# Optimization experiments

Hardware: AMD Instinct MI355X
Metric: run time of the kernel (lower is better)

The kernel has to match this reference:

```python
import jax, jax.numpy as jnp
import numpy as np

LEAKY_SLOPE = 0.2  # LeakyReLU(0.2) attention activation from the torch module
HEADS = 4
RATES = (10, 25)


def _prod(v):
    r = 1
    for x in v:
        r *= x
    return r


def gat_conv(x_self, x_neigh, W, a_s, a_n):
    """Single GAT aggregation layer (aggregate_method='concat').
    x_self:  [..., F_in]
    x_neigh: [..., E, F_in] (leading dims reshape-compatible with x_self)
    W: [F_in, H*D], a_s/a_n: [H, D]
    Returns [..., H*D].
    """
    H = HEADS
    D = W.shape[1] // H
    lead = x_self.shape[:-1]
    E = x_neigh.shape[-2]
    z_s = (x_self @ W).reshape(lead + (H, D))                  # [..., H, D]
    z_n = (x_neigh @ W).reshape(lead + (E, H, D))              # [..., E, H, D]
    e_s = jnp.einsum('...hd,hd->...h', z_s, a_s)               # [..., H]
    e_n = jnp.einsum('...ehd,hd->...eh', z_n, a_n)             # [..., E, H]
    logits = jax.nn.leaky_relu(e_s[..., None, :] + e_n, LEAKY_SLOPE)
    alpha = jax.nn.softmax(logits, axis=-2)                    # softmax over neighbors E
    out = jnp.einsum('...eh,...ehd->...hd', alpha, z_n)        # attention-weighted sum
    return out.reshape(lead + (H * D,))


def setup_inputs() -> dict:
    key = jax.random.key(0)
    ks = jax.random.split(key, 10)
    B, F, HID, OUT = 1024, 128, 512, 256
    s = 0.05
    return {
        'h0': jax.random.normal(ks[0], (B, F), jnp.float32),
        'h1': jax.random.normal(ks[1], (B, RATES[0], F), jnp.float32),
        'h2': jax.random.normal(ks[2], (B, RATES[0] * RATES[1], F), jnp.float32),
        'W0': jax.random.normal(ks[3], (F, HID), jnp.float32) * s,
        'a0_s': jax.random.normal(ks[4], (HEADS, HID // HEADS), jnp.float32) * s,
        'a0_n': jax.random.normal(ks[5], (HEADS, HID // HEADS), jnp.float32) * s,
        'W1': jax.random.normal(ks[6], (HID, HID), jnp.float32) * s,
        'a1_s': jax.random.normal(ks[7], (HEADS, HID // HEADS), jnp.float32) * s,
        'a1_n': jax.random.normal(ks[8], (HEADS, HID // HEADS), jnp.float32) * s,
        'W_fc': jax.random.normal(ks[9], (HID, OUT), jnp.float32) * s,
    }


def reference(h0, h1, h2, W0, a0_s, a0_n, W1, a1_s, a1_n, W_fc):
    B = h0.shape[0]
    hs = [h0, h1, h2]
    layers = [(W0, a0_s, a0_n), (W1, a1_s, a1_n)]
    depth = len(RATES)
    # hierarchical sweep: layer i is applied to levels 0..depth-i-1
    for i, (W, a_s, a_n) in enumerate(layers):
        for j in range(depth - i):
            x_self = hs[j]
            x_neigh = hs[j + 1].reshape(B, _prod(RATES[:j]), RATES[j], -1)
            hs[j] = gat_conv(x_self, x_neigh, W, a_s, a_n)
    return hs[0] @ W_fc  # final Linear (no bias, no activation)
```

## Files before the change

kernel.cpp:

```cpp
#include <hip/hip_runtime.h>

__device__ __forceinline__ void gemm_body(
    float* __restrict__ smem,
    const float* __restrict__ A, int lda,
    const float* __restrict__ B, int ldb,
    float* __restrict__ C, int ldc, int K,
    int m0, int col0) {
  float* As = smem;
  float* Bs = smem + 16 * 68;
  const int t = threadIdx.x;
  const int tn = t & 31, tm = t >> 5;
  const int lam = t >> 2, lak = (t & 3) * 4;
  const int lbk = t >> 4, lbn = (t & 15) * 8;
  float acc[8][4];
#pragma unroll
  for (int i = 0; i < 8; ++i)
#pragma unroll
    for (int j = 0; j < 4; ++j) acc[i][j] = 0.f;
  for (int k0 = 0; k0 < K; k0 += 16) {
    float4 av = *reinterpret_cast<const float4*>(A + (size_t)(m0 + lam) * lda + k0 + lak);
    As[(lak + 0) * 68 + lam] = av.x;
    As[(lak + 1) * 68 + lam] = av.y;
    As[(lak + 2) * 68 + lam] = av.z;
    As[(lak + 3) * 68 + lam] = av.w;
    const float* bp = B + (size_t)(k0 + lbk) * ldb + col0 + lbn;
    float4 b0 = *reinterpret_cast<const float4*>(bp);
    float4 b1 = *reinterpret_cast<const float4*>(bp + 4);
    float* bd = &Bs[lbk * 132 + lbn];
    bd[0] = b0.x; bd[1] = b0.y; bd[2] = b0.z; bd[3] = b0.w;
    bd[4] = b1.x; bd[5] = b1.y; bd[6] = b1.z; bd[7] = b1.w;
    __syncthreads();
#pragma unroll
    for (int kk = 0; kk < 16; ++kk) {
      float4 a0 = *reinterpret_cast<const float4*>(&As[kk * 68 + tm * 8]);
      float4 a1 = *reinterpret_cast<const float4*>(&As[kk * 68 + tm * 8 + 4]);
      float4 bv = *reinterpret_cast<const float4*>(&Bs[kk * 132 + tn * 4]);
      float a[8] = {a0.x, a0.y, a0.z, a0.w, a1.x, a1.y, a1.z, a1.w};
      float b[4] = {bv.x, bv.y, bv.z, bv.w};
#pragma unroll
      for (int i = 0; i < 8; ++i)
#pragma unroll
        for (int j = 0; j < 4; ++j) acc[i][j] = fmaf(a[i], b[j], acc[i][j]);
    }
    __syncthreads();
  }
#pragma unroll
  for (int i = 0; i < 8; ++i) {
    float* cp = C + (size_t)(m0 + tm * 8 + i) * ldc + col0 + tn * 4;
    *reinterpret_cast<float4*>(cp) =
        make_float4(acc[i][0], acc[i][1], acc[i][2], acc[i][3]);
  }
}

template <int FIN, int TPR, int E>
__device__ __forceinline__ void gat_body(
    float* __restrict__ smem,
    const float* __restrict__ xself, const float* __restrict__ xneigh,
    const float* __restrict__ waS, const float* __restrict__ waN,
    float* __restrict__ out) {
  constexpr int MR = E + 1;
  constexpr int RPP = 256 / TPR;
  constexpr int PSTR = TPR + 1;
  constexpr int G = TPR / 4;
  float* tile = smem;
  float* partial = tile + MR * FIN;
  float* logitS = partial + MR * PSTR;
  float* alpha = logitS + MR * 4;
  const int t = threadIdx.x;
  const int el = t / TPR;
  const int f0 = (t % TPR) * 4;
  float4 wn[4], ws[4];
#pragma unroll
  for (int h = 0; h < 4; ++h) {
    wn[h] = *reinterpret_cast<const float4*>(waN + h * FIN + f0);
    ws[h] = *reinterpret_cast<const float4*>(waS + h * FIN + f0);
  }
#pragma unroll
  for (int p = 0; p * RPP < MR; ++p) {
    int e = p * RPP + el;
    if (e < MR) {
      const float* src = (e < E) ? (xneigh + (size_t)e * FIN + f0) : (xself + f0);
      float4 x = *reinterpret_cast<const float4*>(src);
      *reinterpret_cast<float4*>(tile + e * FIN + f0) = x;
      float ph[4];
#pragma unroll
      for (int h = 0; h < 4; ++h) {
        float4 w = (e < E) ? wn[h] : ws[h];
        ph[h] = x.x * w.x + x.y * w.y + x.z * w.z + x.w * w.w;
      }
#pragma unroll
      for (int h = 0; h < 4; ++h) {
        ph[h] += __shfl_xor(ph[h], 1);
        ph[h] += __shfl_xor(ph[h], 2);
      }
      if ((t & 3) == 0) {
        int g = (t % TPR) >> 2;
        *reinterpret_cast<float4*>(partial + e * PSTR + g * 4) =
            make_float4(ph[0], ph[1], ph[2], ph[3]);
      }
    }
  }
  __syncthreads();
  if (t < MR * 4) {
    int e = t >> 2, h = t & 3;
    float v = 0.f;
#pragma unroll
    for (int g = 0; g < G; ++g) v += partial[e * PSTR + g * 4 + h];
    logitS[t] = v;
  }
  __syncthreads();
  if (t < 4) {
    const float es = logitS[E * 4 + t];
    float m = -1e30f;
#pragma unroll
    for (int e = 0; e < E; ++e) {
      float x = es + logitS[e * 4 + t];
      x = (x > 0.f) ? x : 0.2f * x;
      m = fmaxf(m, x);
    }
    float s = 0.f;
#pragma unroll
    for (int e = 0; e < E; ++e) {
      float x = es + logitS[e * 4 + t];
      x = (x > 0.f) ? x : 0.2f * x;
      float p = __expf(x - m);
      alpha[e * 4 + t] = p;
      s += p;
    }
    float inv = 1.f / s;
#pragma unroll
    for (int e = 0; e < E; ++e) alpha[e * 4 + t] *= inv;
  }
  __syncthreads();
  constexpr int C = FIN / 4;
  for (int o = t; o < 4 * C; o += 256) {
    int h = o / C, f = (o % C) * 4;
    float4 acc = make_float4(0.f, 0.f, 0.f, 0.f);
#pragma unroll
    for (int e = 0; e < E; ++e) {
      float a = alpha[e * 4 + h];
      float4 x = *reinterpret_cast<const float4*>(tile + e * FIN + f);
      acc.x = fmaf(a, x.x, acc.x);
      acc.y = fmaf(a, x.y, acc.y);
      acc.z = fmaf(a, x.z, acc.z);
      acc.w = fmaf(a, x.w, acc.w);
    }
    *reinterpret_cast<float4*>(out + h * FIN + f) = acc;
  }
}

__global__ void __launch_bounds__(256) prepA(
    const float* __restrict__ W0, const float* __restrict__ a0s,
    const float* __restrict__ a0n,
    const float* __restrict__ W1, const float* __restrict__ a1s,
    const float* __restrict__ a1n, const float* __restrict__ Wfc,
    float* __restrict__ wa0s, float* __restrict__ wa0n,
    float* __restrict__ wa1s, float* __restrict__ wa1n,
    float* __restrict__ T) {
  __shared__ float smem[3200];
  const int b = blockIdx.x;
  if (b < 64) {
    int h = b >> 4, mb = (b >> 1) & 7, nb = b & 1;
    gemm_body(smem, W1 + h * 128, 512, Wfc + (size_t)h * 32768, 256,
              T + (size_t)h * 131072, 256, 128, mb * 64, nb * 128);
    return;
  }
  int idx = (b - 64) * 256 + threadIdx.x;
  if (idx >= 5120) return;
  const float* W; const float* a; float* dst; int i; int FIN;
  if (idx < 512)       { W = W0; a = a0s; dst = wa0s; i = idx;        FIN = 128; }
  else if (idx < 1024) { W = W0; a = a0n; dst = wa0n; i = idx - 512;  FIN = 128; }
  else if (idx < 3072) { W = W1; a = a1s; dst = wa1s; i = idx - 1024; FIN = 512; }
  else                 { W = W1; a = a1n; dst = wa1n; i = idx - 3072; FIN = 512; }
  int f = i >> 2, h = i & 3;
  const float* wrow = W + (size_t)f * 512 + h * 128;
  const float* arow = a + h * 128;
  float v = 0.f;
#pragma unroll 8
  for (int d = 0; d < 128; ++d) v = fmaf(wrow[d], arow[d], v);
  dst[h * FIN + f] = v;
}

__global__ void __launch_bounds__(256) fusedB(
    const float* __restrict__ h0, const float* __restrict__ h1,
    const float* __restrict__ h2, const float* __restrict__ wa0s,
    const float* __restrict__ wa0n, float* __restrict__ xagg,
    const float* __restrict__ W0, const float* __restrict__ wa1s,
    const float* __restrict__ wa1n, const float* __restrict__ T,
    float* __restrict__ va1s, float* __restrict__ va1n,
    float* __restrict__ Wfinal) {
  __shared__ float smem[4390];
  const int b = blockIdx.x;
  if (b < 1024) {
    gat_body<128, 32, 10>(smem, h0 + (size_t)b * 128, h1 + (size_t)b * 1280,
                          wa0s, wa0n, xagg + (size_t)b * 512);
    return;
  }
  if (b < 11264) {
    int g = b - 1024;
    gat_body<128, 32, 25>(smem, h1 + (size_t)g * 128, h2 + (size_t)g * 3200,
                          wa0s, wa0n, xagg + (size_t)b * 512);
    return;
  }
  if (b < 11264 + 64) {
    int g = b - 11264;
    int pair = g >> 2, mb = (g >> 1) & 1, nb = g & 1;
    int h = pair >> 2, h0b = pair & 3;
    gemm_body(smem, W0 + h0b * 128, 512,
              T + (size_t)h * 131072 + (size_t)h0b * 32768, 256,
              Wfinal + (size_t)h * 131072 + (size_t)h0b * 32768, 256, 128,
              mb * 64, nb * 128);
    return;
  }
  int idx = (b - 11328) * 256 + threadIdx.x;
  if (idx >= 4096) return;
  const float* wa = (idx < 2048) ? wa1s : wa1n;
  float* dst = (idx < 2048) ? va1s : va1n;
  int i = idx & 2047;
  int h = i >> 9, h0b = (i >> 7) & 3, f = i & 127;
  const float* w0row = W0 + (size_t)f * 512 + h0b * 128;
  const float* warow = wa + h * 512 + h0b * 128;
  float v = 0.f;
#pragma unroll 8
  for (int n = 0; n < 128; ++n) v = fmaf(w0row[n], warow[n], v);
  dst[i] = v;
}

__global__ void __launch_bounds__(256) gat_layer1(
    const float* __restrict__ xagg, const float* __restrict__ vaS,
    const float* __restrict__ vaN, float* __restrict__ aggx) {
  __shared__ float smem[7135];
  const int b = blockIdx.x;
  gat_body<512, 128, 10>(smem, xagg + (size_t)b * 512,
                         xagg + (size_t)(1024 + b * 10) * 512, vaS, vaN,
                         aggx + (size_t)b * 2048);
}

__global__ void __launch_bounds__(256) gemm_ksplit(
    const float* __restrict__ A, const float* __restrict__ B,
    float* __restrict__ Cpart) {
  __shared__ float smem[3200];
  const int ks = blockIdx.z;
  gemm_body(smem, A + ks * 256, 2048, B + (size_t)ks * 65536, 256,
            Cpart + (size_t)ks * 262144, 256, 256, blockIdx.x * 64,
            blockIdx.y * 128);
}

__global__ void __launch_bounds__(256) reduce8(
    const float* __restrict__ Cpart, float* __restrict__ out) {
  int i = blockIdx.x * 256 + threadIdx.x;
  const float4* p = reinterpret_cast<const float4*>(Cpart) + i;
  float4 s = p[0];
#pragma unroll
  for (int ks = 1; ks < 8; ++ks) {
    float4 v = p[(size_t)ks * 65536];
    s.x += v.x; s.y += v.y; s.z += v.z; s.w += v.w;
  }
  reinterpret_cast<float4*>(out)[i] = s;
}

extern "C" void kernel_launch(void* const* d_in, const int* in_sizes, int n_in,
                              void* d_out, int out_size, void* d_ws, size_t ws_size,
                              hipStream_t stream) {
  const float* h0  = (const float*)d_in[0];
  const float* h1  = (const float*)d_in[1];
  const float* h2  = (const float*)d_in[2];
  const float* W0  = (const float*)d_in[3];
  const float* a0s = (const float*)d_in[4];
  const float* a0n = (const float*)d_in[5];
  const float* W1  = (const float*)d_in[6];
  const float* a1s = (const float*)d_in[7];
  const float* a1n = (const float*)d_in[8];
  const float* Wfc = (const float*)d_in[9];
  float* out = (float*)d_out;

  float* ws = (float*)d_ws;
  float* wa0s   = ws;
  float* wa0n   = wa0s + 512;
  float* wa1s   = wa0n + 512;
  float* wa1n   = wa1s + 2048;
  float* va1s   = wa1n + 2048;
  float* va1n   = va1s + 2048;
  float* T      = va1n + 2048;
  float* Wfinal = T + 524288;
  float* xaggA  = Wfinal + 524288;
  float* aggx   = xaggA + 11264 * 512;
  float* Cpart  = aggx + 2097152;

  prepA<<<84, 256, 0, stream>>>(W0, a0s, a0n, W1, a1s, a1n, Wfc,
                                wa0s, wa0n, wa1s, wa1n, T);
  fusedB<<<11344, 256, 0, stream>>>(h0, h1, h2, wa0s, wa0n, xaggA,
                                    W0, wa1s, wa1n, T, va1s, va1n, Wfinal);
  gat_layer1<<<1024, 256, 0, stream>>>(xaggA, va1s, va1n, aggx);
  gemm_ksplit<<<dim3(16, 2, 8), 256, 0, stream>>>(aggx, Wfinal, Cpart);
  reduce8<<<256, 256, 0, stream>>>(Cpart, out);
}
```

Measured before the change: 271.5 us.

## Shrink GEMM tiles, use shuffle reductions and parallel softmax in GAT body

The GEMM helper moves from 64x128 to 32x128 tiles, which doubles the block count for the weight-prep and k-split GEMMs and lowers per-thread registers. The GAT attention logits are now fully reduced with warp shuffles instead of a shared-memory partial sum. The softmax runs across 64 threads with shuffle max and sum reductions instead of 4 serial threads. The weighted aggregation uses float2 so more threads take part, and the small GEMM and vector blocks are placed first in the fused launch so they do not wait behind the GAT blocks. Together these aim to cut serial work and LDS usage per block, at the cost of more blocks and less register reuse in the GEMMs.

```diff
diff --git a/kernel.cpp b/kernel.cpp
--- a/kernel.cpp
+++ b/kernel.cpp
@@ -1,52 +1,53 @@
 #include <hip/hip_runtime.h>
 
-__device__ __forceinline__ void gemm_body(
+__device__ __forceinline__ void gemm32(
     float* __restrict__ smem,
     const float* __restrict__ A, int lda,
     const float* __restrict__ B, int ldb,
     float* __restrict__ C, int ldc, int K,
     int m0, int col0) {
   float* As = smem;
-  float* Bs = smem + 16 * 68;
+  float* Bs = smem + 16 * 36;
   const int t = threadIdx.x;
   const int tn = t & 31, tm = t >> 5;
   const int lam = t >> 2, lak = (t & 3) * 4;
   const int lbk = t >> 4, lbn = (t & 15) * 8;
-  float acc[8][4];
-#pragma unroll
-  for (int i = 0; i < 8; ++i)
+  float acc[4][4];
+#pragma unroll
+  for (int i = 0; i < 4; ++i)
 #pragma unroll
     for (int j = 0; j < 4; ++j) acc[i][j] = 0.f;
   for (int k0 = 0; k0 < K; k0 += 16) {
-    float4 av = *reinterpret_cast<const float4*>(A + (size_t)(m0 + lam) * lda + k0 + lak);
-    As[(lak + 0) * 68 + lam] = av.x;
-    As[(lak + 1) * 68 + lam] = av.y;
-    As[(lak + 2) * 68 + lam] = av.z;
-    As[(lak + 3) * 68 + lam] = av.w;
+    if (t < 128) {
+      float4 av = *reinterpret_cast<const float4*>(A + (size_t)(m0 + lam) * lda + k0 + lak);
+      As[(lak + 0) * 36 + lam] = av.x;
+      As[(lak + 1) * 36 + lam] = av.y;
+      As[(lak + 2) * 36 + lam] = av.z;
+      As[(lak + 3) * 36 + lam] = av.w;
+    }
     const float* bp = B + (size_t)(k0 + lbk) * ldb + col0 + lbn;
     float4 b0 = *reinterpret_cast<const float4*>(bp);
     float4 b1 = *reinterpret_cast<const float4*>(bp + 4);
     float* bd = &Bs[lbk * 132 + lbn];
-    bd[0] = b0.x; bd[1] = b0.y; bd[2] = b0.z; bd[3] = b0.w;
-    bd[4] = b1.x; bd[5] = b1.y; bd[6] = b1.z; bd[7] = b1.w;
+    *reinterpret_cast<float4*>(bd) = b0;
+    *reinterpret_cast<float4*>(bd + 4) = b1;
     __syncthreads();
 #pragma unroll
     for (int kk = 0; kk < 16; ++kk) {
-      float4 a0 = *reinterpret_cast<const float4*>(&As[kk * 68 + tm * 8]);
-      float4 a1 = *reinterpret_cast<const float4*>(&As[kk * 68 + tm * 8 + 4]);
-      float4 bv = *reinterpret_cast<const float4*>(&Bs[kk * 132 + tn * 4]);
-      float a[8] = {a0.x, a0.y, a0.z, a0.w, a1.x, a1.y, a1.z, a1.w};
-      float b[4] = {bv.x, bv.y, bv.z, bv.w};
-#pragma unroll
-      for (int i = 0; i < 8; ++i)
+      float4 a4 = *reinterpret_cast<const float4*>(&As[kk * 36 + tm * 4]);
+      float4 b4 = *reinterpret_cast<const float4*>(&Bs[kk * 132 + tn * 4]);
+      float a[4] = {a4.x, a4.y, a4.z, a4.w};
+      float b[4] = {b4.x, b4.y, b4.z, b4.w};
+#pragma unroll
+      for (int i = 0; i < 4; ++i)
 #pragma unroll
         for (int j = 0; j < 4; ++j) acc[i][j] = fmaf(a[i], b[j], acc[i][j]);
     }
     __syncthreads();
   }
 #pragma unroll
-  for (int i = 0; i < 8; ++i) {
-    float* cp = C + (size_t)(m0 + tm * 8 + i) * ldc + col0 + tn * 4;
+  for (int i = 0; i < 4; ++i) {
+    float* cp = C + (size_t)(m0 + tm * 4 + i) * ldc + col0 + tn * 4;
     *reinterpret_cast<float4*>(cp) =
         make_float4(acc[i][0], acc[i][1], acc[i][2], acc[i][3]);
   }
@@ -60,12 +61,10 @@
     float* __restrict__ out) {
   constexpr int MR = E + 1;
   constexpr int RPP = 256 / TPR;
-  constexpr int PSTR = TPR + 1;
-  constexpr int G = TPR / 4;
+  constexpr int PP = (TPR > 64) ? 8 : 4;
   float* tile = smem;
   float* partial = tile + MR * FIN;
-  float* logitS = partial + MR * PSTR;
-  float* alpha = logitS + MR * 4;
+  float* alpha = partial + MR * PP;
   const int t = threadIdx.x;
   const int el = t / TPR;
   const int f0 = (t % TPR) * 4;
@@ -92,60 +91,76 @@
       for (int h = 0; h < 4; ++h) {
         ph[h] += __shfl_xor(ph[h], 1);
         ph[h] += __shfl_xor(ph[h], 2);
+        ph[h] += __shfl_xor(ph[h], 4);
+        ph[h] += __shfl_xor(ph[h], 8);
+        ph[h] += __shfl_xor(ph[h], 16);
+        if constexpr (TPR > 64) ph[h] += __shfl_xor(ph[h], 32);
       }
-      if ((t & 3) == 0) {
-        int g = (t % TPR) >> 2;
-        *reinterpret_cast<float4*>(partial + e * PSTR + g * 4) =
-            make_float4(ph[0], ph[1], ph[2], ph[3]);
+      if constexpr (TPR <= 64) {
+        if ((t & (TPR - 1)) == 0)
+          *reinterpret_cast<float4*>(partial + e * 4) =
+              make_float4(ph[0], ph[1], ph[2], ph[3]);
+      } else {
+        if ((t & 63) == 0) {
+          int half = (t >> 6) & 1;
+          *reinterpret_cast<float4*>(partial + e * 8 + half * 4) =
+              make_float4(ph[0], ph[1], ph[2], ph[3]);
+        }
       }
     }
   }
   __syncthreads();
-  if (t < MR * 4) {
-    int e = t >> 2, h = t & 3;
-    float v = 0.f;
-#pragma unroll
-    for (int g = 0; g < G; ++g) v += partial[e * PSTR + g * 4 + h];
-    logitS[t] = v;
+  if (t < 64) {
+    const int h = t & 3;
+    const int e0 = t >> 2;
+    float selfl = partial[E * PP + h];
+    if constexpr (PP == 8) selfl += partial[E * PP + 4 + h];
+    float x0 = -1e30f, x1 = -1e30f;
+    if (e0 < E) {
+      float v = partial[e0 * PP + h];
+      if constexpr (PP == 8) v += partial[e0 * PP + 4 + h];
+      float x = selfl + v;
+      x0 = (x > 0.f) ? x : 0.2f * x;
+    }
+    if constexpr (E > 16) {
+      if (e0 + 16 < E) {
+        float v = partial[(e0 + 16) * PP + h];
+        if constexpr (PP == 8) v += partial[(e0 + 16) * PP + 4 + h];
+        float x = selfl + v;
+        x1 = (x > 0.f) ? x : 0.2f * x;
+      }
+    }
+    float m = fmaxf(x0, x1);
+    m = fmaxf(m, __shfl_xor(m, 4));
+    m = fmaxf(m, __shfl_xor(m, 8));
+    m = fmaxf(m, __shfl_xor(m, 16));
+    m = fmaxf(m, __shfl_xor(m, 32));
+    float p0 = (e0 < E) ? __expf(x0 - m) : 0.f;
+    float p1 = 0.f;
+    if constexpr (E > 16) p1 = (e0 + 16 < E) ? __expf(x1 - m) : 0.f;
+    float s = p0 + p1;
+    s += __shfl_xor(s, 4);
+    s += __shfl_xor(s, 8);
+    s += __shfl_xor(s, 16);
+    s += __shfl_xor(s, 32);
+    float inv = 1.f / s;
+    if (e0 < E) alpha[e0 * 4 + h] = p0 * inv;
+    if constexpr (E > 16)
+      if (e0 + 16 < E) alpha[(e0 + 16) * 4 + h] = p1 * inv;
   }
   __syncthreads();
-  if (t < 4) {
-    const float es = logitS[E * 4 + t];
-    float m = -1e30f;
-#pragma unroll
-    for (int e = 0; e < E; ++e) {
-      float x = es + logitS[e * 4 + t];
-      x = (x > 0.f) ? x : 0.2f * x;
-      m = fmaxf(m, x);
-    }
-    float s = 0.f;
-#pragma unroll
-    for (int e = 0; e < E; ++e) {
-      float x = es + logitS[e * 4 + t];
-      x = (x > 0.f) ? x : 0.2f * x;
-      float p = __expf(x - m);
-      alpha[e * 4 + t] = p;
-      s += p;
-    }
-    float inv = 1.f / s;
-#pragma unroll
-    for (int e = 0; e < E; ++e) alpha[e * 4 + t] *= inv;
-  }
-  __syncthreads();
-  constexpr int C = FIN / 4;
-  for (int o = t; o < 4 * C; o += 256) {
-    int h = o / C, f = (o % C) * 4;
-    float4 acc = make_float4(0.f, 0.f, 0.f, 0.f);
+  constexpr int C2 = FIN / 2;
+  for (int o = t; o < 4 * C2; o += 256) {
+    int h = o / C2, f = (o % C2) * 2;
+    float2 acc = make_float2(0.f, 0.f);
 #pragma unroll
     for (int e = 0; e < E; ++e) {
       float a = alpha[e * 4 + h];
-      float4 x = *reinterpret_cast<const float4*>(tile + e * FIN + f);
+      float2 x = *reinterpret_cast<const float2*>(tile + e * FIN + f);
       acc.x = fmaf(a, x.x, acc.x);
       acc.y = fmaf(a, x.y, acc.y);
-      acc.z = fmaf(a, x.z, acc.z);
-      acc.w = fmaf(a, x.w, acc.w);
-    }
-    *reinterpret_cast<float4*>(out + h * FIN + f) = acc;
+    }
+    *reinterpret_cast<float2*>(out + h * FIN + f) = acc;
   }
 }
 
@@ -157,15 +172,15 @@
     float* __restrict__ wa0s, float* __restrict__ wa0n,
     float* __restrict__ wa1s, float* __restrict__ wa1n,
     float* __restrict__ T) {
-  __shared__ float smem[3200];
+  __shared__ float smem[2688];
   const int b = blockIdx.x;
-  if (b < 64) {
-    int h = b >> 4, mb = (b >> 1) & 7, nb = b & 1;
-    gemm_body(smem, W1 + h * 128, 512, Wfc + (size_t)h * 32768, 256,
-              T + (size_t)h * 131072, 256, 128, mb * 64, nb * 128);
+  if (b < 128) {
+    int h = b >> 5, mb = (b >> 1) & 15, nb = b & 1;
+    gemm32(smem, W1 + h * 128, 512, Wfc + (size_t)h * 32768, 256,
+           T + (size_t)h * 131072, 256, 128, mb * 32, nb * 128);
     return;
   }
-  int idx = (b - 64) * 256 + threadIdx.x;
+  int idx = (b - 128) * 256 + threadIdx.x;
   if (idx >= 5120) return;
   const float* W; const float* a; float* dst; int i; int FIN;
   if (idx < 512)       { W = W0; a = a0s; dst = wa0s; i = idx;        FIN = 128; }
@@ -189,47 +204,45 @@
     const float* __restrict__ wa1n, const float* __restrict__ T,
     float* __restrict__ va1s, float* __restrict__ va1n,
     float* __restrict__ Wfinal) {
-  __shared__ float smem[4390];
+  __shared__ float smem[3532];
   const int b = blockIdx.x;
-  if (b < 1024) {
-    gat_body<128, 32, 10>(smem, h0 + (size_t)b * 128, h1 + (size_t)b * 1280,
-                          wa0s, wa0n, xagg + (size_t)b * 512);
+  if (b < 128) {
+    int h = b >> 5, h0b = (b >> 3) & 3, mb = (b >> 1) & 3, nb = b & 1;
+    gemm32(smem, W0 + h0b * 128, 512,
+           T + (size_t)h * 131072 + (size_t)h0b * 32768, 256,
+           Wfinal + (size_t)h * 131072 + (size_t)h0b * 32768, 256, 128,
+           mb * 32, nb * 128);
     return;
   }
-  if (b < 11264) {
-    int g = b - 1024;
-    gat_body<128, 32, 25>(smem, h1 + (size_t)g * 128, h2 + (size_t)g * 3200,
-                          wa0s, wa0n, xagg + (size_t)b * 512);
+  if (b < 144) {
+    int idx = (b - 128) * 256 + threadIdx.x;
+    const float* wa = (idx < 2048) ? wa1s : wa1n;
+    float* dst = (idx < 2048) ? va1s : va1n;
+    int i = idx & 2047;
+    int h = i >> 9, h0b = (i >> 7) & 3, f = i & 127;
+    const float* w0row = W0 + (size_t)f * 512 + h0b * 128;
+    const float* warow = wa + h * 512 + h0b * 128;
+    float v = 0.f;
+#pragma unroll 8
+    for (int n = 0; n < 128; ++n) v = fmaf(w0row[n], warow[n], v);
+    dst[i] = v;
     return;
   }
-  if (b < 11264 + 64) {
-    int g = b - 11264;
-    int pair = g >> 2, mb = (g >> 1) & 1, nb = g & 1;
-    int h = pair >> 2, h0b = pair & 3;
-    gemm_body(smem, W0 + h0b * 128, 512,
-              T + (size_t)h * 131072 + (size_t)h0b * 32768, 256,
-              Wfinal + (size_t)h * 131072 + (size_t)h0b * 32768, 256, 128,
-              mb * 64, nb * 128);
+  if (b < 144 + 1024) {
+    int n = b - 144;
+    gat_body<128, 32, 10>(smem, h0 + (size_t)n * 128, h1 + (size_t)n * 1280,
+                          wa0s, wa0n, xagg + (size_t)n * 512);
     return;
   }
-  int idx = (b - 11328) * 256 + threadIdx.x;
-  if (idx >= 4096) return;
-  const float* wa = (idx < 2048) ? wa1s : wa1n;
-  float* dst = (idx < 2048) ? va1s : va1n;
-  int i = idx & 2047;
-  int h = i >> 9, h0b = (i >> 7) & 3, f = i & 127;
-  const float* w0row = W0 + (size_t)f * 512 + h0b * 128;
-  const float* warow = wa + h * 512 + h0b * 128;
-  float v = 0.f;
-#pragma unroll 8
-  for (int n = 0; n < 128; ++n) v = fmaf(w0row[n], warow[n], v);
-  dst[i] = v;
+  int g = b - 1168;
+  gat_body<128, 32, 25>(smem, h1 + (size_t)g * 128, h2 + (size_t)g * 3200,
+                        wa0s, wa0n, xagg + (size_t)(1024 + g) * 512);
 }
 
 __global__ void __launch_bounds__(256) gat_layer1(
     const float* __restrict__ xagg, const float* __restrict__ vaS,
     const float* __restrict__ vaN, float* __restrict__ aggx) {
-  __shared__ float smem[7135];
+  __shared__ float smem[5760];
   const int b = blockIdx.x;
   gat_body<512, 128, 10>(smem, xagg + (size_t)b * 512,
                          xagg + (size_t)(1024 + b * 10) * 512, vaS, vaN,
@@ -239,11 +252,11 @@
 __global__ void __launch_bounds__(256) gemm_ksplit(
     const float* __restrict__ A, const float* __restrict__ B,
     float* __restrict__ Cpart) {
-  __shared__ float smem[3200];
+  __shared__ float smem[2688];
   const int ks = blockIdx.z;
-  gemm_body(smem, A + ks * 256, 2048, B + (size_t)ks * 65536, 256,
-            Cpart + (size_t)ks * 262144, 256, 256, blockIdx.x * 64,
-            blockIdx.y * 128);
+  gemm32(smem, A + ks * 256, 2048, B + (size_t)ks * 65536, 256,
+         Cpart + (size_t)ks * 262144, 256, 256, blockIdx.x * 32,
+         blockIdx.y * 128);
 }
 
 __global__ void __launch_bounds__(256) reduce8(
@@ -287,11 +300,11 @@
   float* aggx   = xaggA + 11264 * 512;
   float* Cpart  = aggx + 2097152;
 
-  prepA<<<84, 256, 0, stream>>>(W0, a0s, a0n, W1, a1s, a1n, Wfc,
-                                wa0s, wa0n, wa1s, wa1n, T);
-  fusedB<<<11344, 256, 0, stream>>>(h0, h1, h2, wa0s, wa0n, xaggA,
+  prepA<<<148, 256, 0, stream>>>(W0, a0s, a0n, W1, a1s, a1n, Wfc,
+                                 wa0s, wa0n, wa1s, wa1n, T);
+  fusedB<<<11408, 256, 0, stream>>>(h0, h1, h2, wa0s, wa0n, xaggA,
                                     W0, wa1s, wa1n, T, va1s, va1n, Wfinal);
   gat_layer1<<<1024, 256, 0, stream>>>(xaggA, va1s, va1n, aggx);
-  gemm_ksplit<<<dim3(16, 2, 8), 256, 0, stream>>>(aggx, Wfinal, Cpart);
+  gemm_ksplit<<<dim3(32, 2, 8), 256, 0, stream>>>(aggx, Wfinal, Cpart);
   reduce8<<<256, 256, 0, stream>>>(Cpart, out);
 }
```

Measured after the change: 263.7 us. 2.9% less time.
